# Kernel optimization log

Hardware: AMD Instinct MI355X
Metric: run time of the kernel (lower is better)

## Reference

```python
import jax, jax.numpy as jnp
import numpy as np

N_NODES = 50000
N_EDGES = 800000
N_GRAPHS = 256
DIMS = [64, 128, 256, 512]
GRU_H = 256


def _linit(key, shape, fan_in):
    lim = 1.0 / np.sqrt(fan_in)
    return jax.random.uniform(key, shape, jnp.float32, -lim, lim)


def setup_inputs() -> dict:
    key = jax.random.key(0)
    ks = jax.random.split(key, 24)
    x = jax.random.normal(ks[0], (N_NODES, DIMS[0]), jnp.float32)
    edge_index = jax.random.randint(ks[1], (2, N_EDGES), 0, N_NODES, jnp.int64)
    batch_idx = jnp.sort(jax.random.randint(ks[2], (N_NODES,), 0, N_GRAPHS, jnp.int64))
    inp = {"x": x, "edge_index": edge_index, "batch_idx": batch_idx}
    # GCN layer weights (stored [in, out]) and biases
    for i in range(3):
        inp[f"gcn_w{i}"] = _linit(ks[3 + i], (DIMS[i], DIMS[i + 1]), DIMS[i])
        inp[f"gcn_b{i}"] = jnp.zeros((DIMS[i + 1],), jnp.float32)
    # gate nn: Linear(512, 1)
    inp["gate_w"] = _linit(ks[6], (DIMS[3], 1), DIMS[3])
    inp["gate_b"] = jnp.zeros((1,), jnp.float32)
    # GRU: 2 layers, torch layout W_ih [3H, in], W_hh [3H, H]
    ins = [DIMS[3], GRU_H]
    for l in range(2):
        inp[f"gru_wih{l}"] = _linit(ks[7 + 4 * l], (3 * GRU_H, ins[l]), GRU_H)
        inp[f"gru_whh{l}"] = _linit(ks[8 + 4 * l], (3 * GRU_H, GRU_H), GRU_H)
        inp[f"gru_bih{l}"] = _linit(ks[9 + 4 * l], (3 * GRU_H,), GRU_H)
        inp[f"gru_bhh{l}"] = _linit(ks[10 + 4 * l], (3 * GRU_H,), GRU_H)
    # output proj: Linear(256, 512), torch layout [out, in]
    inp["proj_w"] = _linit(ks[15], (DIMS[3], GRU_H), GRU_H)
    inp["proj_b"] = jnp.zeros((DIMS[3],), jnp.float32)
    return inp


def _gcn_norm(edge_index, n_nodes):
    # add self-loops, symmetric normalization (PyG GCNConv default)
    loop = jnp.arange(n_nodes, dtype=edge_index.dtype)
    src = jnp.concatenate([edge_index[0], loop])
    dst = jnp.concatenate([edge_index[1], loop])
    deg = jax.ops.segment_sum(jnp.ones_like(dst, jnp.float32), dst, num_segments=n_nodes)
    dinv = jnp.where(deg > 0, jax.lax.rsqrt(jnp.maximum(deg, 1.0)), 0.0)
    norm = dinv[src] * dinv[dst]
    return src, dst, norm


def _gru_cell(xv, h, wih, whh, bih, bhh):
    gi = xv @ wih.T + bih
    gh = h @ whh.T + bhh
    ir, iz, inn = jnp.split(gi, 3, axis=-1)
    hr, hz, hn = jnp.split(gh, 3, axis=-1)
    r = jax.nn.sigmoid(ir + hr)
    z = jax.nn.sigmoid(iz + hz)
    n = jnp.tanh(inn + r * hn)
    return (1.0 - z) * n + z * h


def reference(x, edge_index, batch_idx,
              gcn_w0, gcn_b0, gcn_w1, gcn_b1, gcn_w2, gcn_b2,
              gate_w, gate_b,
              gru_wih0, gru_whh0, gru_bih0, gru_bhh0,
              gru_wih1, gru_whh1, gru_bih1, gru_bhh1,
              proj_w, proj_b):
    n = x.shape[0]
    src, dst, norm = _gcn_norm(edge_index, n)
    for w, b in ((gcn_w0, gcn_b0), (gcn_w1, gcn_b1), (gcn_w2, gcn_b2)):
        h = x @ w                                  # [N, out]
        msg = h[src] * norm[:, None]               # gather over edges
        x = jax.ops.segment_sum(msg, dst, num_segments=n) + b
        x = jax.nn.relu(x)
    # attentional aggregation: segment softmax over gate scores
    gate = (x @ gate_w + gate_b)[:, 0]             # [N]
    gmax = jax.ops.segment_max(gate, batch_idx, num_segments=N_GRAPHS)
    e = jnp.exp(gate - gmax[batch_idx])
    denom = jax.ops.segment_sum(e, batch_idx, num_segments=N_GRAPHS)
    alpha = e / denom[batch_idx]
    graph_emb = jax.ops.segment_sum(x * alpha[:, None], batch_idx, num_segments=N_GRAPHS)  # [G, 512]
    # 2-layer GRU with seq_len=1, h0=0
    h0 = jnp.zeros((N_GRAPHS, GRU_H), x.dtype)
    h1 = _gru_cell(graph_emb, h0, gru_wih0, gru_whh0, gru_bih0, gru_bhh0)
    h2 = _gru_cell(h1, h0, gru_wih1, gru_whh1, gru_bih1, gru_bhh1)
    return h2 @ proj_w.T + proj_b                  # [G, 512]
```

## Files before the change

kernel.cpp:

```cpp
#include <hip/hip_runtime.h>


#define N_GRAPHS 256
#define GRU_H 256
#define SCAN_CHUNK 2048

typedef __attribute__((ext_vector_type(8))) short short8;
typedef __attribute__((ext_vector_type(4))) float floatx4;

typedef unsigned short ushort_t;
typedef unsigned int uint_t;

__device__ __forceinline__ float bflo(uint_t u) { return __uint_as_float(u << 16); }
__device__ __forceinline__ float bfhi(uint_t u) { return __uint_as_float(u & 0xffff0000u); }
__device__ __forceinline__ uint_t f2bf(float f) {
    uint_t u = __float_as_uint(f);
    return (u + 0x7fffu + ((u >> 16) & 1u)) >> 16;
}
__device__ __forceinline__ uint_t pack2(float a, float b) {
    return f2bf(a) | (f2bf(b) << 16);
}


__global__ void k_hist(const int* __restrict__ dst, int* __restrict__ counts, int E) {
    int e = blockIdx.x * blockDim.x + threadIdx.x;
    if (e < E) atomicAdd(&counts[dst[e]], 1);
}

__global__ __launch_bounds__(256) void k_scan1(const int* __restrict__ counts,
                                               int* __restrict__ rowptr,
                                               int* __restrict__ bpre,
                                               int* __restrict__ bsums,
                                               float* __restrict__ dinv, int n) {
    int b = blockIdx.x, t = threadIdx.x;
    int base = b * SCAN_CHUNK + t * 8;
    int v[8];
    int s = 0;
#pragma unroll
    for (int j = 0; j < 8; ++j) {
        int i = base + j;
        int c = (i < n) ? counts[i] : 0;
        v[j] = s;
        s += c;
        if (i < n) dinv[i] = rsqrtf((float)(c + 1));
    }
    __shared__ int sd[256];
    sd[t] = s;
    __syncthreads();
    for (int off = 1; off < 256; off <<= 1) {
        int tmp = (t >= off) ? sd[t - off] : 0;
        __syncthreads();
        sd[t] += tmp;
        __syncthreads();
    }
    int texcl = sd[t] - s;
    if (t == 255) bsums[b] = sd[255];
#pragma unroll
    for (int j = 0; j < 8; ++j) {
        int i = base + j;
        if (i < n) {
            rowptr[i] = texcl + v[j];
            bpre[i] = (j < 7) ? (texcl + v[j + 1]) : sd[t];
        }
    }
}

__global__ __launch_bounds__(256) void k_scan3(int* __restrict__ rowptr,
                                               int* __restrict__ cursor,
                                               const int* __restrict__ bpre,
                                               int* __restrict__ bcur,
                                               const int* __restrict__ bsums,
                                               int n, int nb) {
    int b = blockIdx.x, t = threadIdx.x;
    __shared__ int s_off;
    if (t == 0) {
        int off = 0, tot = 0;
        for (int i = 0; i < nb; ++i) {
            int v = bsums[i];
            if (i < b) off += v;
            tot += v;
        }
        s_off = off;
        if (b == 0) rowptr[n] = tot;
    }
    __syncthreads();
    int off = s_off;
    int base = b * SCAN_CHUNK + t * 8;
#pragma unroll
    for (int j = 0; j < 8; ++j) {
        int i = base + j;
        if (i < n) {
            int r = rowptr[i] + off;
            rowptr[i] = r;
            cursor[i] = r;
            bcur[i] = bpre[i] + off;
        }
    }
}


__global__ __launch_bounds__(256) void k_pack(
    const int* __restrict__ src, const int* __restrict__ dst,
    int* __restrict__ cursor, int* __restrict__ bcur, int S,
    int* __restrict__ col, int E,
    const float4* __restrict__ x, const float* __restrict__ dinv,
    uint4* __restrict__ xs, int N,
    const float* __restrict__ w0, const float* __restrict__ w1,
    const float* __restrict__ w2, ushort_t* __restrict__ wt0,
    ushort_t* __restrict__ wt1, ushort_t* __restrict__ wt2,
    const float* __restrict__ wih0, const float* __restrict__ wih1,
    const float* __restrict__ pw,
    ushort_t* __restrict__ sh0, ushort_t* __restrict__ sl0,
    ushort_t* __restrict__ sh1, ushort_t* __restrict__ sl1,
    ushort_t* __restrict__ sh2, ushort_t* __restrict__ sl2,
    int nf, int np, int nw) {
    int b = blockIdx.x, t = threadIdx.x;
    if (b < nf) {
        int ebase = b * 2048 + t * 8;
        if (ebase + 8 <= E) {
            int4 s0 = *(const int4*)(src + ebase);
            int4 s1 = *(const int4*)(src + ebase + 4);
            int4 d0 = *(const int4*)(dst + ebase);
            int4 d1 = *(const int4*)(dst + ebase + 4);
            int ss[8] = {s0.x, s0.y, s0.z, s0.w, s1.x, s1.y, s1.z, s1.w};
            int dd[8] = {d0.x, d0.y, d0.z, d0.w, d1.x, d1.y, d1.z, d1.w};
            int pos[8];
#pragma unroll
            for (int j = 0; j < 8; ++j)
                pos[j] = (ss[j] < S) ? atomicAdd(&cursor[dd[j]], 1)
                                     : atomicAdd(&bcur[dd[j]], -1) - 1;
#pragma unroll
            for (int j = 0; j < 8; ++j) col[pos[j]] = ss[j];
        } else {
#pragma unroll
            for (int j = 0; j < 8; ++j) {
                int e = ebase + j;
                if (e < E) {
                    int d = dst[e], s = src[e];
                    int pos = (s < S) ? atomicAdd(&cursor[d], 1)
                                      : atomicAdd(&bcur[d], -1) - 1;
                    col[pos] = s;
                }
            }
        }
    } else if (b < nf + np) {
        int idx = (b - nf) * 256 + t;
        int n = idx >> 3;
        if (n < N) {
            float dn = dinv[n];
            float4 v0 = x[idx * 2], v1 = x[idx * 2 + 1];
            uint4 o;
            o.x = pack2(v0.x * dn, v0.y * dn);
            o.y = pack2(v0.z * dn, v0.w * dn);
            o.z = pack2(v1.x * dn, v1.y * dn);
            o.w = pack2(v1.z * dn, v1.w * dn);
            xs[idx] = o;
        }
    } else if (b < nf + np + nw) {
        int idx = (b - nf - np) * 256 + t;
        if (idx < 8192) {
            int k = idx >> 7, n = idx & 127;
            wt0[(size_t)n * 64 + k] = (ushort_t)f2bf(w0[idx]);
        } else if (idx < 40960) {
            int i = idx - 8192;
            int k = i >> 8, n = i & 255;
            wt1[(size_t)n * 128 + k] = (ushort_t)f2bf(w1[i]);
        } else if (idx < 172032) {
            int i = idx - 40960;
            int k = i >> 9, n = i & 511;
            wt2[(size_t)n * 256 + k] = (ushort_t)f2bf(w2[i]);
        }
    } else {
        int idx = (b - nf - np - nw) * 256 + t;
        const float* s; ushort_t* H; ushort_t* L; int i;
        if (idx < 393216)      { s = wih0; H = sh0; L = sl0; i = idx; }
        else if (idx < 589824) { s = wih1; H = sh1; L = sl1; i = idx - 393216; }
        else if (idx < 720896) { s = pw;   H = sh2; L = sl2; i = idx - 589824; }
        else return;
        float v = s[i];
        uint_t h = f2bf(v);
        H[i] = (ushort_t)h;
        L[i] = (ushort_t)f2bf(v - __uint_as_float(h << 16));
    }
}


__device__ __forceinline__ void acc8(float& a0, float& a1, float& a2, float& a3,
                                     float& a4, float& a5, float& a6, float& a7,
                                     const uint4& v) {
    a0 += bflo(v.x); a1 += bfhi(v.x); a2 += bflo(v.y); a3 += bfhi(v.y);
    a4 += bflo(v.z); a5 += bfhi(v.z); a6 += bflo(v.w); a7 += bfhi(v.w);
}

__global__ void k_gather_bf16(const uint4* __restrict__ xs, const int* __restrict__ rp,
                              const int* __restrict__ col, const float* __restrict__ dinv,
                              uint4* __restrict__ agg, int N, int shift ) {
    int idx = blockIdx.x * blockDim.x + threadIdx.x;
    int n = idx >> shift;
    if (n >= N) return;
    int c = idx & ((1 << shift) - 1);
    int C8 = 1 << shift;
    int a = rp[n], b = rp[n + 1];
    uint4 u = xs[(size_t)n * C8 + c];
    float a0 = bflo(u.x), a1 = bfhi(u.x), a2 = bflo(u.y), a3 = bfhi(u.y);
    float a4 = bflo(u.z), a5 = bfhi(u.z), a6 = bflo(u.w), a7 = bfhi(u.w);
    int k = a;
    for (; k + 8 <= b; k += 8) {
        int ci[8];
#pragma unroll
        for (int j = 0; j < 8; ++j) ci[j] = col[k + j];
        uint4 v[8];
#pragma unroll
        for (int j = 0; j < 8; ++j) v[j] = xs[(size_t)ci[j] * C8 + c];
#pragma unroll
        for (int j = 0; j < 8; ++j)
            acc8(a0, a1, a2, a3, a4, a5, a6, a7, v[j]);
    }
    for (; k + 4 <= b; k += 4) {
        int ci[4];
#pragma unroll
        for (int j = 0; j < 4; ++j) ci[j] = col[k + j];
        uint4 v[4];
#pragma unroll
        for (int j = 0; j < 4; ++j) v[j] = xs[(size_t)ci[j] * C8 + c];
#pragma unroll
        for (int j = 0; j < 4; ++j)
            acc8(a0, a1, a2, a3, a4, a5, a6, a7, v[j]);
    }
    for (; k < b; ++k) {
        uint4 v = xs[(size_t)col[k] * C8 + c];
        acc8(a0, a1, a2, a3, a4, a5, a6, a7, v);
    }
    float dn = dinv[n];
    uint4 o;
    o.x = pack2(a0 * dn, a1 * dn);
    o.y = pack2(a2 * dn, a3 * dn);
    o.z = pack2(a4 * dn, a5 * dn);
    o.w = pack2(a6 * dn, a7 * dn);
    agg[idx] = o;
}


__global__ __launch_bounds__(256) void k_gather_split(
    const uint4* __restrict__ xsP, const int* __restrict__ rp,
    const int* __restrict__ split, const int* __restrict__ col,
    const float* __restrict__ dinv, uint4* __restrict__ agg,
    int N, int c8shift , int lgshift ,
    int half, int dstChunk) {
    int id = blockIdx.x;
    int x = id & 7;
    int q = x & ((1 << lgshift) - 1);
    int dg = x >> lgshift;
    int nb = id >> 3;
    int t = threadIdx.x;
    int n = dg * dstChunk + nb * 32 + (t >> 3);
    if (n >= N || n >= (dg + 1) * dstChunk) return;
    int lane8 = t & 7;
    const uint4* plane = xsP + (size_t)q * (size_t)N * 8;
    size_t outOff = ((size_t)n << c8shift) + (q << 3) + lane8;
    int a = half ? split[n] : rp[n];
    int b = half ? rp[n + 1] : split[n];
    float a0, a1, a2, a3, a4, a5, a6, a7;
    uint4 prev;
    if (half) {
        prev = agg[outOff];
        a0 = a1 = a2 = a3 = a4 = a5 = a6 = a7 = 0.f;
    } else {
        uint4 u = plane[(size_t)n * 8 + lane8];
        a0 = bflo(u.x); a1 = bfhi(u.x); a2 = bflo(u.y); a3 = bfhi(u.y);
        a4 = bflo(u.z); a5 = bfhi(u.z); a6 = bflo(u.w); a7 = bfhi(u.w);
    }
    int k = a;
    for (; k + 8 <= b; k += 8) {
        int ci[8];
#pragma unroll
        for (int j = 0; j < 8; ++j) ci[j] = col[k + j];
        uint4 v[8];
#pragma unroll
        for (int j = 0; j < 8; ++j) v[j] = plane[(size_t)ci[j] * 8 + lane8];
#pragma unroll
        for (int j = 0; j < 8; ++j)
            acc8(a0, a1, a2, a3, a4, a5, a6, a7, v[j]);
    }
    for (; k + 4 <= b; k += 4) {
        int ci[4];
#pragma unroll
        for (int j = 0; j < 4; ++j) ci[j] = col[k + j];
        uint4 v[4];
#pragma unroll
        for (int j = 0; j < 4; ++j) v[j] = plane[(size_t)ci[j] * 8 + lane8];
#pragma unroll
        for (int j = 0; j < 4; ++j)
            acc8(a0, a1, a2, a3, a4, a5, a6, a7, v[j]);
    }
    for (; k < b; ++k) {
        uint4 v = plane[(size_t)col[k] * 8 + lane8];
        acc8(a0, a1, a2, a3, a4, a5, a6, a7, v);
    }
    float dn = dinv[n];
    uint4 o;
    if (half) {
        o.x = pack2(bflo(prev.x) + a0 * dn, bfhi(prev.x) + a1 * dn);
        o.y = pack2(bflo(prev.y) + a2 * dn, bfhi(prev.y) + a3 * dn);
        o.z = pack2(bflo(prev.z) + a4 * dn, bfhi(prev.z) + a5 * dn);
        o.w = pack2(bflo(prev.w) + a6 * dn, bfhi(prev.w) + a7 * dn);
    } else {
        o.x = pack2(a0 * dn, a1 * dn);
        o.y = pack2(a2 * dn, a3 * dn);
        o.z = pack2(a4 * dn, a5 * dn);
        o.w = pack2(a6 * dn, a7 * dn);
    }
    agg[outOff] = o;
}


__global__ __launch_bounds__(256) void k_gemm_mfma(
    const ushort_t* __restrict__ A, const ushort_t* __restrict__ Wt,
    const float* __restrict__ bias, const float* __restrict__ dinv,
    ushort_t* __restrict__ C, int M, int K, int Nout, int scale_out,
    const float* __restrict__ gate_w, float* __restrict__ gateArr,
    int mB, int bnShift, int planeC) {
    int id = blockIdx.x;
    int xcd = id & 7;
    int k2 = id >> 3;
    int bnI = k2 & ((1 << bnShift) - 1);
    int bmI = (k2 >> bnShift) * 8 + xcd;
    if (bmI >= mB) return;
    int bm = bmI * 64, bn = bnI * 64;

    __shared__ ushort_t As[64 * 72];
    __shared__ ushort_t Bs[64 * 72];
    int tid = threadIdx.x;
    int wave = tid >> 6, lane = tid & 63;
    int quad = lane >> 4, lr = lane & 15;
    int wm = (wave & 1) * 32, wn = (wave >> 1) * 32;

    floatx4 zero = {0.f, 0.f, 0.f, 0.f};
    floatx4 acc00 = zero, acc01 = zero, acc10 = zero, acc11 = zero;

    int r0 = tid >> 3,         ko0 = (tid & 7) * 8;
    int r1 = (tid + 256) >> 3, ko1 = ((tid + 256) & 7) * 8;

    for (int k0 = 0; k0 < K; k0 += 64) {
        int ar0 = min(bm + r0, M - 1);
        int ar1 = min(bm + r1, M - 1);
        uint4 av0 = *(const uint4*)(A + (size_t)ar0 * K + k0 + ko0);
        uint4 av1 = *(const uint4*)(A + (size_t)ar1 * K + k0 + ko1);
        uint4 bv0 = *(const uint4*)(Wt + (size_t)(bn + r0) * K + k0 + ko0);
        uint4 bv1 = *(const uint4*)(Wt + (size_t)(bn + r1) * K + k0 + ko1);
        __syncthreads();
        *(uint4*)&As[r0 * 72 + ko0] = av0;
        *(uint4*)&As[r1 * 72 + ko1] = av1;
        *(uint4*)&Bs[r0 * 72 + ko0] = bv0;
        *(uint4*)&Bs[r1 * 72 + ko1] = bv1;
        __syncthreads();
#pragma unroll
        for (int ks = 0; ks < 2; ++ks) {
            short8 af0 = *(short8*)&As[(wm + lr) * 72 + ks * 32 + quad * 8];
            short8 af1 = *(short8*)&As[(wm + 16 + lr) * 72 + ks * 32 + quad * 8];
            short8 bf0 = *(short8*)&Bs[(wn + lr) * 72 + ks * 32 + quad * 8];
            short8 bf1 = *(short8*)&Bs[(wn + 16 + lr) * 72 + ks * 32 + quad * 8];
            acc00 = __builtin_amdgcn_mfma_f32_16x16x32_bf16(af0, bf0, acc00, 0, 0, 0);
            acc01 = __builtin_amdgcn_mfma_f32_16x16x32_bf16(af0, bf1, acc01, 0, 0, 0);
            acc10 = __builtin_amdgcn_mfma_f32_16x16x32_bf16(af1, bf0, acc10, 0, 0, 0);
            acc11 = __builtin_amdgcn_mfma_f32_16x16x32_bf16(af1, bf1, acc11, 0, 0, 0);
        }
    }

    float gwv[2] = {0.f, 0.f};
    if (gate_w) {
        gwv[0] = gate_w[bn + wn + lr];
        gwv[1] = gate_w[bn + wn + 16 + lr];
    }
    size_t m64 = (size_t)M * 64;
    float pg[2][4] = {};
#pragma unroll
    for (int mi = 0; mi < 2; ++mi) {
#pragma unroll
        for (int ni = 0; ni < 2; ++ni) {
            floatx4 acc = (mi == 0) ? (ni == 0 ? acc00 : acc01)
                                    : (ni == 0 ? acc10 : acc11);
            int col = bn + wn + ni * 16 + lr;
            float bcol = bias[col];
#pragma unroll
            for (int r = 0; r < 4; ++r) {
                int row = bm + wm + mi * 16 + quad * 4 + r;
                if (row < M) {
                    float v = acc[r] + bcol;
                    v = fmaxf(v, 0.0f);
                    if (gate_w) pg[mi][r] += v * gwv[ni];
                    if (scale_out) v *= dinv[row];
                    size_t cidx = planeC
                        ? (size_t)(col >> 6) * m64 + (size_t)row * 64 + (col & 63)
                        : (size_t)row * Nout + col;
                    C[cidx] = (ushort_t)f2bf(v);
                }
            }
        }
    }
    if (gate_w) {
#pragma unroll
        for (int mi = 0; mi < 2; ++mi) {
#pragma unroll
            for (int r = 0; r < 4; ++r) {
                float p = pg[mi][r];
                p += __shfl_down(p, 8, 16);
                p += __shfl_down(p, 4, 16);
                p += __shfl_down(p, 2, 16);
                p += __shfl_down(p, 1, 16);
                if (lr == 0) {
                    int row = bm + wm + mi * 16 + quad * 4 + r;
                    if (row < M) atomicAdd(&gateArr[row], p);
                }
            }
        }
    }
}


__global__ __launch_bounds__(256) void k_gemm3(
    const ushort_t* __restrict__ Ahi, const ushort_t* __restrict__ Alo,
    const ushort_t* __restrict__ Whi, const ushort_t* __restrict__ Wlo,
    const float* __restrict__ bias, float* __restrict__ C,
    int M, int K, int Nout) {
    __shared__ ushort_t AsH[64 * 72];
    __shared__ ushort_t AsL[64 * 72];
    __shared__ ushort_t BsH[64 * 72];
    __shared__ ushort_t BsL[64 * 72];
    int tid = threadIdx.x;
    int wave = tid >> 6, lane = tid & 63;
    int quad = lane >> 4, lr = lane & 15;
    int wm = (wave & 1) * 32, wn = (wave >> 1) * 32;
    int bm = blockIdx.x * 64, bn = blockIdx.y * 64;

    floatx4 zero = {0.f, 0.f, 0.f, 0.f};
    floatx4 acc00 = zero, acc01 = zero, acc10 = zero, acc11 = zero;

    int r0 = tid >> 3,         ko0 = (tid & 7) * 8;
    int r1 = (tid + 256) >> 3, ko1 = ((tid + 256) & 7) * 8;

    for (int k0 = 0; k0 < K; k0 += 64) {
        int ar0 = min(bm + r0, M - 1);
        int ar1 = min(bm + r1, M - 1);
        size_t a0o = (size_t)ar0 * K + k0 + ko0, a1o = (size_t)ar1 * K + k0 + ko1;
        size_t b0o = (size_t)(bn + r0) * K + k0 + ko0, b1o = (size_t)(bn + r1) * K + k0 + ko1;
        uint4 ah0 = *(const uint4*)(Ahi + a0o), ah1 = *(const uint4*)(Ahi + a1o);
        uint4 al0 = *(const uint4*)(Alo + a0o), al1 = *(const uint4*)(Alo + a1o);
        uint4 bh0 = *(const uint4*)(Whi + b0o), bh1 = *(const uint4*)(Whi + b1o);
        uint4 bl0 = *(const uint4*)(Wlo + b0o), bl1 = *(const uint4*)(Wlo + b1o);
        __syncthreads();
        *(uint4*)&AsH[r0 * 72 + ko0] = ah0; *(uint4*)&AsH[r1 * 72 + ko1] = ah1;
        *(uint4*)&AsL[r0 * 72 + ko0] = al0; *(uint4*)&AsL[r1 * 72 + ko1] = al1;
        *(uint4*)&BsH[r0 * 72 + ko0] = bh0; *(uint4*)&BsH[r1 * 72 + ko1] = bh1;
        *(uint4*)&BsL[r0 * 72 + ko0] = bl0; *(uint4*)&BsL[r1 * 72 + ko1] = bl1;
        __syncthreads();
#pragma unroll
        for (int ks = 0; ks < 2; ++ks) {
            int a0i = (wm + lr) * 72 + ks * 32 + quad * 8;
            int a1i = (wm + 16 + lr) * 72 + ks * 32 + quad * 8;
            int b0i = (wn + lr) * 72 + ks * 32 + quad * 8;
            int b1i = (wn + 16 + lr) * 72 + ks * 32 + quad * 8;
            short8 afh0 = *(short8*)&AsH[a0i], afh1 = *(short8*)&AsH[a1i];
            short8 afl0 = *(short8*)&AsL[a0i], afl1 = *(short8*)&AsL[a1i];
            short8 bfh0 = *(short8*)&BsH[b0i], bfh1 = *(short8*)&BsH[b1i];
            short8 bfl0 = *(short8*)&BsL[b0i], bfl1 = *(short8*)&BsL[b1i];
            acc00 = __builtin_amdgcn_mfma_f32_16x16x32_bf16(afh0, bfh0, acc00, 0, 0, 0);
            acc00 = __builtin_amdgcn_mfma_f32_16x16x32_bf16(afh0, bfl0, acc00, 0, 0, 0);
            acc00 = __builtin_amdgcn_mfma_f32_16x16x32_bf16(afl0, bfh0, acc00, 0, 0, 0);
            acc01 = __builtin_amdgcn_mfma_f32_16x16x32_bf16(afh0, bfh1, acc01, 0, 0, 0);
            acc01 = __builtin_amdgcn_mfma_f32_16x16x32_bf16(afh0, bfl1, acc01, 0, 0, 0);
            acc01 = __builtin_amdgcn_mfma_f32_16x16x32_bf16(afl0, bfh1, acc01, 0, 0, 0);
            acc10 = __builtin_amdgcn_mfma_f32_16x16x32_bf16(afh1, bfh0, acc10, 0, 0, 0);
            acc10 = __builtin_amdgcn_mfma_f32_16x16x32_bf16(afh1, bfl0, acc10, 0, 0, 0);
            acc10 = __builtin_amdgcn_mfma_f32_16x16x32_bf16(afl1, bfh0, acc10, 0, 0, 0);
            acc11 = __builtin_amdgcn_mfma_f32_16x16x32_bf16(afh1, bfh1, acc11, 0, 0, 0);
            acc11 = __builtin_amdgcn_mfma_f32_16x16x32_bf16(afh1, bfl1, acc11, 0, 0, 0);
            acc11 = __builtin_amdgcn_mfma_f32_16x16x32_bf16(afl1, bfh1, acc11, 0, 0, 0);
        }
    }

#pragma unroll
    for (int mi = 0; mi < 2; ++mi) {
#pragma unroll
        for (int ni = 0; ni < 2; ++ni) {
            floatx4 acc = (mi == 0) ? (ni == 0 ? acc00 : acc01)
                                    : (ni == 0 ? acc10 : acc11);
            int col = bn + wn + ni * 16 + lr;
            float bcol = bias ? bias[col] : 0.0f;
#pragma unroll
            for (int r = 0; r < 4; ++r) {
                int row = bm + wm + mi * 16 + quad * 4 + r;
                if (row < M)
                    C[(size_t)row * Nout + col] = acc[r] + bcol;
            }
        }
    }
}


__global__ void k_gru_ep(const float* __restrict__ gi, const float* __restrict__ bih,
                         const float* __restrict__ bhh,
                         ushort_t* __restrict__ hhi, ushort_t* __restrict__ hlo, int G) {
    int idx = blockIdx.x * blockDim.x + threadIdx.x;
    int g = idx >> 8, j = idx & 255;
    if (g >= G) return;
    const float* row = gi + (size_t)g * 768;
    float ir = row[j]       + bih[j]       + bhh[j];
    float iz = row[j + 256] + bih[j + 256] + bhh[j + 256];
    float in = row[j + 512] + bih[j + 512];
    float r = 1.0f / (1.0f + expf(-ir));
    float z = 1.0f / (1.0f + expf(-iz));
    float nn = tanhf(in + r * bhh[j + 512]);
    float h = (1.0f - z) * nn;
    uint_t hi = f2bf(h);
    hhi[idx] = (ushort_t)hi;
    hlo[idx] = (ushort_t)f2bf(h - __uint_as_float(hi << 16));
}


__global__ __launch_bounds__(256) void k_softmax_emb(
    const uint_t* __restrict__ x , const float* __restrict__ gate,
    const int* __restrict__ batch, int N,
    ushort_t* __restrict__ embH, ushort_t* __restrict__ embL) {
    int g = blockIdx.x;
    int s, e;
    {
        int lo = 0, hi = N;
        while (lo < hi) { int mid = (lo + hi) >> 1; if (batch[mid] < g) lo = mid + 1; else hi = mid; }
        s = lo;
        lo = s; hi = N;
        while (lo < hi) { int mid = (lo + hi) >> 1; if (batch[mid] < g + 1) lo = mid + 1; else hi = mid; }
        e = lo;
    }
    __shared__ float red[256];
    __shared__ float sal[256];
    int tid = threadIdx.x;
    float m = -INFINITY;
    for (int i = s + tid; i < e; i += 256) m = fmaxf(m, gate[i]);
    red[tid] = m; __syncthreads();
    for (int off = 128; off > 0; off >>= 1) {
        if (tid < off) red[tid] = fmaxf(red[tid], red[tid + off]);
        __syncthreads();
    }
    m = red[0]; __syncthreads();
    float ssum = 0.f;
    for (int i = s + tid; i < e; i += 256) ssum += expf(gate[i] - m);
    red[tid] = ssum; __syncthreads();
    for (int off = 128; off > 0; off >>= 1) {
        if (tid < off) red[tid] += red[tid + off];
        __syncthreads();
    }
    float denom = red[0];
    float inv = (denom > 0.f) ? 1.0f / denom : 0.0f;
    float acc0 = 0.f, acc1 = 0.f;
    for (int base = s; base < e; base += 256) {
        int i = base + tid;
        __syncthreads();
        sal[tid] = (i < e) ? expf(gate[i] - m) * inv : 0.0f;
        __syncthreads();
        int cnt = min(256, e - base);
        for (int k = 0; k < cnt; ++k) {
            float a = sal[k];
            uint_t u = x[(size_t)(base + k) * 256 + tid];
            acc0 += a * bflo(u);
            acc1 += a * bfhi(u);
        }
    }
    int i0 = g * 512 + tid * 2;
    uint_t h0 = f2bf(acc0);
    uint_t h1 = f2bf(acc1);
    embH[i0]     = (ushort_t)h0;
    embH[i0 + 1] = (ushort_t)h1;
    embL[i0]     = (ushort_t)f2bf(acc0 - __uint_as_float(h0 << 16));
    embL[i0 + 1] = (ushort_t)f2bf(acc1 - __uint_as_float(h1 << 16));
}


extern "C" void kernel_launch(void* const* d_in, const int* in_sizes, int n_in,
                              void* d_out, int out_size, void* d_ws, size_t ws_size,
                              hipStream_t stream) {
    const float* x       = (const float*)d_in[0];
    const int*   ei      = (const int*)d_in[1];
    const int*   batch   = (const int*)d_in[2];
    const float* w0      = (const float*)d_in[3];
    const float* b0      = (const float*)d_in[4];
    const float* w1      = (const float*)d_in[5];
    const float* b1      = (const float*)d_in[6];
    const float* w2      = (const float*)d_in[7];
    const float* b2      = (const float*)d_in[8];
    const float* gate_w  = (const float*)d_in[9];
    const float* wih0    = (const float*)d_in[11];
    const float* bih0    = (const float*)d_in[13];
    const float* bhh0    = (const float*)d_in[14];
    const float* wih1    = (const float*)d_in[15];
    const float* bih1    = (const float*)d_in[17];
    const float* bhh1    = (const float*)d_in[18];
    const float* pw      = (const float*)d_in[19];
    const float* pb      = (const float*)d_in[20];
    float* out = (float*)d_out;

    const int N = in_sizes[2];
    const int E = in_sizes[1] / 2;
    const int G = N_GRAPHS;

    char* base = (char*)d_ws;
    size_t off = 0;
    auto alloc = [&](size_t bytes) -> char* {
        char* p = base + off;
        off = (off + bytes + 255) & ~(size_t)255;
        return p;
    };
    ushort_t* bufA  = (ushort_t*)alloc((size_t)N * 512 * 2);
    ushort_t* bufB  = (ushort_t*)alloc((size_t)N * 512 * 2);
    float* dinv     = (float*)alloc((size_t)N * 4);
    float* gateArr  = (float*)alloc((size_t)N * 4);
    int*   counts   = (int*)alloc((size_t)(N + 1) * 4);
    int*   cursor   = (int*)alloc((size_t)(N + 1) * 4);
    int*   bpre     = (int*)alloc((size_t)(N + 1) * 4);
    int*   bcur     = (int*)alloc((size_t)(N + 1) * 4);
    int*   rowptr   = (int*)alloc((size_t)(N + 1) * 4);
    int*   bsums    = (int*)alloc((size_t)256 * 4);
    int*   col      = (int*)alloc((size_t)E * 4);
    ushort_t* wt0   = (ushort_t*)alloc((size_t)128 * 64 * 2);
    ushort_t* wt1   = (ushort_t*)alloc((size_t)256 * 128 * 2);
    ushort_t* wt2   = (ushort_t*)alloc((size_t)512 * 256 * 2);
    ushort_t* ih0H  = (ushort_t*)alloc((size_t)768 * 512 * 2);
    ushort_t* ih0L  = (ushort_t*)alloc((size_t)768 * 512 * 2);
    ushort_t* ih1H  = (ushort_t*)alloc((size_t)768 * 256 * 2);
    ushort_t* ih1L  = (ushort_t*)alloc((size_t)768 * 256 * 2);
    ushort_t* pwH   = (ushort_t*)alloc((size_t)512 * 256 * 2);
    ushort_t* pwL   = (ushort_t*)alloc((size_t)512 * 256 * 2);
    ushort_t* embH  = (ushort_t*)alloc((size_t)G * 512 * 2);
    ushort_t* embL  = (ushort_t*)alloc((size_t)G * 512 * 2);
    ushort_t* h1H   = (ushort_t*)alloc((size_t)G * 256 * 2);
    ushort_t* h1L   = (ushort_t*)alloc((size_t)G * 256 * 2);
    ushort_t* h2H   = (ushort_t*)alloc((size_t)G * 256 * 2);
    ushort_t* h2L   = (ushort_t*)alloc((size_t)G * 256 * 2);
    float* gi       = (float*)alloc((size_t)G * 768 * 4);
    (void)ws_size; (void)n_in; (void)out_size;

    const int* src = ei;
    const int* dst = ei + E;

    const int nb = (N + SCAN_CHUNK - 1) / SCAN_CHUNK;
    const int S = N >> 1;

    size_t zbytes = (size_t)((char*)counts - (char*)gateArr) + (size_t)(N + 1) * 4;
    hipMemsetAsync(gateArr, 0, zbytes, stream);

    k_hist<<<(E + 255) / 256, 256, 0, stream>>>(dst, counts, E);
    k_scan1<<<nb, 256, 0, stream>>>(counts, rowptr, bpre, bsums, dinv, N);
    k_scan3<<<nb, 256, 0, stream>>>(rowptr, cursor, bpre, bcur, bsums, N, nb);

    int nf = (E + 2047) / 2048;
    int np = (N * 8 + 255) / 256;
    int nw = (172032 + 255) / 256;
    int ns = (720896 + 255) / 256;
    k_pack<<<nf + np + nw + ns, 256, 0, stream>>>(
        src, dst, cursor, bcur, S, col, E,
        (const float4*)x, dinv, (uint4*)bufA, N,
        w0, w1, w2, wt0, wt1, wt2,
        wih0, wih1, pw, ih0H, ih0L, ih1H, ih1L, pwH, pwL,
        nf, np, nw);

    int mB = (N + 63) / 64;
    int mBpad = ((mB + 7) / 8) * 8;

    k_gather_bf16<<<(N * 8 + 255) / 256, 256, 0, stream>>>((const uint4*)bufA, rowptr, col, dinv, (uint4*)bufB, N, 3);
    k_gemm_mfma<<<mBpad * 2, 256, 0, stream>>>(bufB, wt0, b0, dinv, bufA, N, 64, 128, 1, nullptr, nullptr, mB, 1, 1);

    int dc2 = (N + 3) / 4;
    int g2 = ((dc2 + 31) / 32) * 8;
    k_gather_split<<<g2, 256, 0, stream>>>((const uint4*)bufA, rowptr, cursor, col, dinv, (uint4*)bufB, N, 4, 1, 0, dc2);
    k_gather_split<<<g2, 256, 0, stream>>>((const uint4*)bufA, rowptr, cursor, col, dinv, (uint4*)bufB, N, 4, 1, 1, dc2);
    k_gemm_mfma<<<mBpad * 4, 256, 0, stream>>>(bufB, wt1, b1, dinv, bufA, N, 128, 256, 1, nullptr, nullptr, mB, 2, 1);

    int dc3 = (N + 1) / 2;
    int g3 = ((dc3 + 31) / 32) * 8;
    k_gather_split<<<g3, 256, 0, stream>>>((const uint4*)bufA, rowptr, cursor, col, dinv, (uint4*)bufB, N, 5, 2, 0, dc3);
    k_gather_split<<<g3, 256, 0, stream>>>((const uint4*)bufA, rowptr, cursor, col, dinv, (uint4*)bufB, N, 5, 2, 1, dc3);
    k_gemm_mfma<<<mBpad * 8, 256, 0, stream>>>(bufB, wt2, b2, dinv, bufA, N, 256, 512, 0, gate_w, gateArr, mB, 3, 0);

    k_softmax_emb<<<G, 256, 0, stream>>>((const uint_t*)bufA, gateArr, batch, N, embH, embL);

    k_gemm3<<<dim3(G / 64, 12), 256, 0, stream>>>(embH, embL, ih0H, ih0L, nullptr, gi, G, 512, 768);
    k_gru_ep<<<G, 256, 0, stream>>>(gi, bih0, bhh0, h1H, h1L, G);

    k_gemm3<<<dim3(G / 64, 12), 256, 0, stream>>>(h1H, h1L, ih1H, ih1L, nullptr, gi, G, 256, 768);
    k_gru_ep<<<G, 256, 0, stream>>>(gi, bih1, bhh1, h2H, h2L, G);

    k_gemm3<<<dim3(G / 64, 8), 256, 0, stream>>>(h2H, h2L, pwH, pwL, pb, out, G, 256, 512);
}
```

Before: 442.1 us.

## Bucket CSR columns into four source quartiles and stage GEMM output through LDS

The CSR build now histograms edges per (source quartile, destination) and scatters them into four ordered sub-ranges per row. Previously edges were split two ways using a forward cursor and a backward cursor, so ordering within each half was arbitrary. The finer source ordering is meant to improve gather locality, while the split-gather kernels keep their two-pass half split via a new split array. Separately, the MFMA GEMM epilogue writes bf16 results to shared memory and then issues coalesced 16-byte global stores instead of scattered 2-byte stores, at the cost of an extra barrier and four times the counter memory.

```diff
diff --git a/kernel.cpp b/kernel.cpp
--- a/kernel.cpp
+++ b/kernel.cpp
@@ -22,14 +22,34 @@
 }
 
 
-__global__ void k_hist(const int* __restrict__ dst, int* __restrict__ counts, int E) {
-    int e = blockIdx.x * blockDim.x + threadIdx.x;
-    if (e < E) atomicAdd(&counts[dst[e]], 1);
+__global__ void k_hist(const int* __restrict__ src, const int* __restrict__ dst,
+                       int* __restrict__ counts, int E, int N,
+                       int T1, int T2, int T3) {
+    int ebase = (blockIdx.x * blockDim.x + threadIdx.x) * 4;
+    if (ebase + 4 <= E) {
+        int4 s4 = *(const int4*)(src + ebase);
+        int4 d4 = *(const int4*)(dst + ebase);
+        int ss[4] = {s4.x, s4.y, s4.z, s4.w};
+        int dd[4] = {d4.x, d4.y, d4.z, d4.w};
+#pragma unroll
+        for (int j = 0; j < 4; ++j) {
+            int q = (ss[j] >= T1) + (ss[j] >= T2) + (ss[j] >= T3);
+            atomicAdd(&counts[q * N + dd[j]], 1);
+        }
+    } else {
+        for (int j = 0; j < 4; ++j) {
+            int e = ebase + j;
+            if (e < E) {
+                int s = src[e];
+                int q = (s >= T1) + (s >= T2) + (s >= T3);
+                atomicAdd(&counts[q * N + dst[e]], 1);
+            }
+        }
+    }
 }
 
 __global__ __launch_bounds__(256) void k_scan1(const int* __restrict__ counts,
                                                int* __restrict__ rowptr,
-                                               int* __restrict__ bpre,
                                                int* __restrict__ bsums,
                                                float* __restrict__ dinv, int n) {
     int b = blockIdx.x, t = threadIdx.x;
@@ -39,10 +59,13 @@
 #pragma unroll
     for (int j = 0; j < 8; ++j) {
         int i = base + j;
-        int c = (i < n) ? counts[i] : 0;
+        int c = 0;
+        if (i < n) {
+            c = counts[i] + counts[n + i] + counts[2 * n + i] + counts[3 * n + i];
+            dinv[i] = rsqrtf((float)(c + 1));
+        }
         v[j] = s;
         s += c;
-        if (i < n) dinv[i] = rsqrtf((float)(c + 1));
     }
     __shared__ int sd[256];
     sd[t] = s;
@@ -58,17 +81,14 @@
 #pragma unroll
     for (int j = 0; j < 8; ++j) {
         int i = base + j;
-        if (i < n) {
-            rowptr[i] = texcl + v[j];
-            bpre[i] = (j < 7) ? (texcl + v[j + 1]) : sd[t];
-        }
+        if (i < n) rowptr[i] = texcl + v[j];
     }
 }
 
 __global__ __launch_bounds__(256) void k_scan3(int* __restrict__ rowptr,
-                                               int* __restrict__ cursor,
-                                               const int* __restrict__ bpre,
-                                               int* __restrict__ bcur,
+                                               const int* __restrict__ counts,
+                                               int* __restrict__ qcur,
+                                               int* __restrict__ split,
                                                const int* __restrict__ bsums,
                                                int n, int nb) {
     int b = blockIdx.x, t = threadIdx.x;
@@ -92,8 +112,12 @@
         if (i < n) {
             int r = rowptr[i] + off;
             rowptr[i] = r;
-            cursor[i] = r;
-            bcur[i] = bpre[i] + off;
+            int c0 = counts[i], c1 = counts[n + i], c2 = counts[2 * n + i];
+            qcur[i]         = r;
+            qcur[n + i]     = r + c0;
+            qcur[2 * n + i] = r + c0 + c1;
+            qcur[3 * n + i] = r + c0 + c1 + c2;
+            split[i]        = r + c0 + c1;
         }
     }
 }
@@ -101,7 +125,7 @@
 
 __global__ __launch_bounds__(256) void k_pack(
     const int* __restrict__ src, const int* __restrict__ dst,
-    int* __restrict__ cursor, int* __restrict__ bcur, int S,
+    int* __restrict__ qcur, int T1, int T2, int T3,
     int* __restrict__ col, int E,
     const float4* __restrict__ x, const float* __restrict__ dinv,
     uint4* __restrict__ xs, int N,
@@ -126,9 +150,10 @@
             int dd[8] = {d0.x, d0.y, d0.z, d0.w, d1.x, d1.y, d1.z, d1.w};
             int pos[8];
 #pragma unroll
-            for (int j = 0; j < 8; ++j)
-                pos[j] = (ss[j] < S) ? atomicAdd(&cursor[dd[j]], 1)
-                                     : atomicAdd(&bcur[dd[j]], -1) - 1;
+            for (int j = 0; j < 8; ++j) {
+                int q = (ss[j] >= T1) + (ss[j] >= T2) + (ss[j] >= T3);
+                pos[j] = atomicAdd(&qcur[q * N + dd[j]], 1);
+            }
 #pragma unroll
             for (int j = 0; j < 8; ++j) col[pos[j]] = ss[j];
         } else {
@@ -136,9 +161,9 @@
             for (int j = 0; j < 8; ++j) {
                 int e = ebase + j;
                 if (e < E) {
-                    int d = dst[e], s = src[e];
-                    int pos = (s < S) ? atomicAdd(&cursor[d], 1)
-                                      : atomicAdd(&bcur[d], -1) - 1;
+                    int s = src[e];
+                    int q = (s >= T1) + (s >= T2) + (s >= T3);
+                    int pos = atomicAdd(&qcur[q * N + dst[e]], 1);
                     col[pos] = s;
                 }
             }
@@ -367,12 +392,13 @@
         }
     }
 
+    __syncthreads();
+    ushort_t* Cs = As;
     float gwv[2] = {0.f, 0.f};
     if (gate_w) {
         gwv[0] = gate_w[bn + wn + lr];
         gwv[1] = gate_w[bn + wn + 16 + lr];
     }
-    size_t m64 = (size_t)M * 64;
     float pg[2][4] = {};
 #pragma unroll
     for (int mi = 0; mi < 2; ++mi) {
@@ -380,21 +406,20 @@
         for (int ni = 0; ni < 2; ++ni) {
             floatx4 acc = (mi == 0) ? (ni == 0 ? acc00 : acc01)
                                     : (ni == 0 ? acc10 : acc11);
-            int col = bn + wn + ni * 16 + lr;
-            float bcol = bias[col];
+            int cc = wn + ni * 16 + lr;
+            float bcol = bias[bn + cc];
 #pragma unroll
             for (int r = 0; r < 4; ++r) {
-                int row = bm + wm + mi * 16 + quad * 4 + r;
+                int rr = wm + mi * 16 + quad * 4 + r;
+                int row = bm + rr;
+                float v = 0.0f;
                 if (row < M) {
-                    float v = acc[r] + bcol;
+                    v = acc[r] + bcol;
                     v = fmaxf(v, 0.0f);
                     if (gate_w) pg[mi][r] += v * gwv[ni];
                     if (scale_out) v *= dinv[row];
-                    size_t cidx = planeC
-                        ? (size_t)(col >> 6) * m64 + (size_t)row * 64 + (col & 63)
-                        : (size_t)row * Nout + col;
-                    C[cidx] = (ushort_t)f2bf(v);
                 }
+                Cs[rr * 72 + cc] = (ushort_t)f2bf(v);
             }
         }
     }
@@ -412,6 +437,24 @@
                     int row = bm + wm + mi * 16 + quad * 4 + r;
                     if (row < M) atomicAdd(&gateArr[row], p);
                 }
+            }
+        }
+    }
+    __syncthreads();
+    {
+        size_t m64 = (size_t)M * 64;
+        int rr = tid >> 2;
+        int cbase = (tid & 3) * 2;
+        int grow = bm + rr;
+        if (grow < M) {
+#pragma unroll
+            for (int c2 = 0; c2 < 2; ++c2) {
+                int chunk = cbase + c2;
+                uint4 v = *(const uint4*)&Cs[rr * 72 + chunk * 8];
+                size_t cidx = planeC
+                    ? (size_t)(bn >> 6) * m64 + (size_t)grow * 64 + chunk * 8
+                    : (size_t)grow * Nout + bn + chunk * 8;
+                *(uint4*)&C[cidx] = v;
             }
         }
     }
@@ -614,10 +657,9 @@
     ushort_t* bufB  = (ushort_t*)alloc((size_t)N * 512 * 2);
     float* dinv     = (float*)alloc((size_t)N * 4);
     float* gateArr  = (float*)alloc((size_t)N * 4);
-    int*   counts   = (int*)alloc((size_t)(N + 1) * 4);
-    int*   cursor   = (int*)alloc((size_t)(N + 1) * 4);
-    int*   bpre     = (int*)alloc((size_t)(N + 1) * 4);
-    int*   bcur     = (int*)alloc((size_t)(N + 1) * 4);
+    int*   counts   = (int*)alloc((size_t)4 * N * 4);
+    int*   qcur     = (int*)alloc((size_t)4 * N * 4);
+    int*   split    = (int*)alloc((size_t)N * 4);
     int*   rowptr   = (int*)alloc((size_t)(N + 1) * 4);
     int*   bsums    = (int*)alloc((size_t)256 * 4);
     int*   col      = (int*)alloc((size_t)E * 4);
@@ -643,21 +685,21 @@
     const int* dst = ei + E;
 
     const int nb = (N + SCAN_CHUNK - 1) / SCAN_CHUNK;
-    const int S = N >> 1;
-
-    size_t zbytes = (size_t)((char*)counts - (char*)gateArr) + (size_t)(N + 1) * 4;
+    const int T1 = N >> 2, T2 = N >> 1, T3 = (N >> 1) + (N >> 2);
+
+    size_t zbytes = (size_t)((char*)qcur - (char*)gateArr);
     hipMemsetAsync(gateArr, 0, zbytes, stream);
 
-    k_hist<<<(E + 255) / 256, 256, 0, stream>>>(dst, counts, E);
-    k_scan1<<<nb, 256, 0, stream>>>(counts, rowptr, bpre, bsums, dinv, N);
-    k_scan3<<<nb, 256, 0, stream>>>(rowptr, cursor, bpre, bcur, bsums, N, nb);
+    k_hist<<<(E + 1023) / 1024, 256, 0, stream>>>(src, dst, counts, E, N, T1, T2, T3);
+    k_scan1<<<nb, 256, 0, stream>>>(counts, rowptr, bsums, dinv, N);
+    k_scan3<<<nb, 256, 0, stream>>>(rowptr, counts, qcur, split, bsums, N, nb);
 
     int nf = (E + 2047) / 2048;
     int np = (N * 8 + 255) / 256;
     int nw = (172032 + 255) / 256;
     int ns = (720896 + 255) / 256;
     k_pack<<<nf + np + nw + ns, 256, 0, stream>>>(
-        src, dst, cursor, bcur, S, col, E,
+        src, dst, qcur, T1, T2, T3, col, E,
         (const float4*)x, dinv, (uint4*)bufA, N,
         w0, w1, w2, wt0, wt1, wt2,
         wih0, wih1, pw, ih0H, ih0L, ih1H, ih1L, pwH, pwL,
@@ -671,14 +713,14 @@
 
     int dc2 = (N + 3) / 4;
     int g2 = ((dc2 + 31) / 32) * 8;
-    k_gather_split<<<g2, 256, 0, stream>>>((const uint4*)bufA, rowptr, cursor, col, dinv, (uint4*)bufB, N, 4, 1, 0, dc2);
-    k_gather_split<<<g2, 256, 0, stream>>>((const uint4*)bufA, rowptr, cursor, col, dinv, (uint4*)bufB, N, 4, 1, 1, dc2);
+    k_gather_split<<<g2, 256, 0, stream>>>((const uint4*)bufA, rowptr, split, col, dinv, (uint4*)bufB, N, 4, 1, 0, dc2);
+    k_gather_split<<<g2, 256, 0, stream>>>((const uint4*)bufA, rowptr, split, col, dinv, (uint4*)bufB, N, 4, 1, 1, dc2);
     k_gemm_mfma<<<mBpad * 4, 256, 0, stream>>>(bufB, wt1, b1, dinv, bufA, N, 128, 256, 1, nullptr, nullptr, mB, 2, 1);
 
     int dc3 = (N + 1) / 2;
     int g3 = ((dc3 + 31) / 32) * 8;
-    k_gather_split<<<g3, 256, 0, stream>>>((const uint4*)bufA, rowptr, cursor, col, dinv, (uint4*)bufB, N, 5, 2, 0, dc3);
-    k_gather_split<<<g3, 256, 0, stream>>>((const uint4*)bufA, rowptr, cursor, col, dinv, (uint4*)bufB, N, 5, 2, 1, dc3);
+    k_gather_split<<<g3, 256, 0, stream>>>((const uint4*)bufA, rowptr, split, col, dinv, (uint4*)bufB, N, 5, 2, 0, dc3);
+    k_gather_split<<<g3, 256, 0, stream>>>((const uint4*)bufA, rowptr, split, col, dinv, (uint4*)bufB, N, 5, 2, 1, dc3);
     k_gemm_mfma<<<mBpad * 8, 256, 0, stream>>>(bufB, wt2, b2, dinv, bufA, N, 256, 512, 0, gate_w, gateArr, mB, 3, 0);
 
     k_softmax_emb<<<G, 256, 0, stream>>>((const uint_t*)bufA, gateArr, batch, N, embH, embL);
```

New measurement: 433.2 us. -2.0%, faster.
